# Kernel tuning notes

Hardware: AMD Instinct MI355X
Metric: run time of the kernel (lower is better)

## Reference

```python
import jax, jax.numpy as jnp
import numpy as np

B = 1024      # batch
E = 1024      # encoding_dim
OUT = 34      # 17 joints x 2 coords


def setup_inputs() -> dict:
    key = jax.random.key(0)
    ks = jax.random.split(key, 8)
    s = 0.02  # weight init scale
    return {
        "h": jax.random.normal(ks[0], (B, E), dtype=jnp.float32),
        "c": jax.random.normal(ks[1], (B, E), dtype=jnp.float32),
        "W_ih": jax.random.normal(ks[2], (4 * E, E), dtype=jnp.float32) * s,
        "W_hh": jax.random.normal(ks[3], (4 * E, E), dtype=jnp.float32) * s,
        "b_ih": jax.random.normal(ks[4], (4 * E,), dtype=jnp.float32) * s,
        "b_hh": jax.random.normal(ks[5], (4 * E,), dtype=jnp.float32) * s,
        "W_out": jax.random.normal(ks[6], (OUT, E), dtype=jnp.float32) * s,
        "b_out": jax.random.normal(ks[7], (OUT,), dtype=jnp.float32) * s,
        "future_preds": 10,
    }


def reference(h, c, W_ih, W_hh, b_ih, b_hh, W_out, b_out, future_preds):
    E_ = h.shape[1]
    start = jnp.zeros_like(h)  # zeros=True start token

    def step(carry, _):
        h_t, c_t, x = carry
        # LSTMCell: gates in PyTorch order i, f, g, o
        gates = x @ W_ih.T + b_ih + h_t @ W_hh.T + b_hh  # [B, 4E]
        i = jax.nn.sigmoid(gates[:, 0 * E_:1 * E_])
        f = jax.nn.sigmoid(gates[:, 1 * E_:2 * E_])
        g = jnp.tanh(gates[:, 2 * E_:3 * E_])
        o = jax.nn.sigmoid(gates[:, 3 * E_:4 * E_])
        c_new = f * c_t + i * g
        h_new = o * jnp.tanh(c_new)
        return (h_new, c_new, h_new), h_new

    _, hs = jax.lax.scan(step, (h, c, start), None, length=future_preds)
    # hs: [T, B, E] -> [B, T, E]
    preds = jnp.transpose(hs, (1, 0, 2))
    return preds @ W_out.T + b_out  # [B, T, 34]
```

## Files before the change

kernel.cpp:

```cpp
#include <hip/hip_runtime.h>
#include <cstdint>
#include <cstddef>

#define E_DIM   1024
#define B_DIM   1024
#define T_STEPS 10
#define OUT_DIM 34
#define OUT_PAD 48
#define HSTR    24
#define EK      128
#define WE_ELEMS (64 * EK)
#define DYN_LDS (2 * WE_ELEMS * 2 + 128 * HSTR * 2)
#define LDP     40

typedef __attribute__((ext_vector_type(4))) float  f32x4;
typedef __attribute__((ext_vector_type(8))) __bf16 bf16x8;

__device__ __forceinline__ unsigned short f2bf(float f) {
    unsigned int u = __float_as_uint(f);
    u = (u + 0x7FFFu + ((u >> 16) & 1u)) >> 16;
    return (unsigned short)u;
}
__device__ __forceinline__ float sigmoid_(float x) { return 1.0f / (1.0f + __expf(-x)); }
__device__ __forceinline__ float tanh_(float x)    { return 2.0f / (1.0f + __expf(-2.0f * x)) - 1.0f; }

__global__ void prep_weights_frag(const float* __restrict__ W_ih, const float* __restrict__ W_hh,
                                  unsigned short* __restrict__ WsumF, unsigned short* __restrict__ WhhF) {
    const int bn = blockIdx.x >> 3, E = blockIdx.x & 7;
    const int nt = threadIdx.x >> 6, lane = threadIdx.x & 63;
    const int j = lane & 15, q = lane >> 4;
    const int srow = nt * E_DIM + bn * 16 + j;
    const float* wi = W_ih + (size_t)srow * E_DIM;
    const float* wh = W_hh + (size_t)srow * E_DIM;
    const size_t dstb = (size_t)bn * 65536 + (size_t)E * 8192 + nt * 512 + lane * 8;
#pragma unroll
    for (int ks8 = 0; ks8 < 4; ++ks8) {
        const int k = E * 128 + ks8 * 32 + q * 8;
        float4 i0 = *(const float4*)(wi + k);
        float4 i1 = *(const float4*)(wi + k + 4);
        float4 h0 = *(const float4*)(wh + k);
        float4 h1 = *(const float4*)(wh + k + 4);
        unsigned short s[8], hh[8];
        s[0] = f2bf(i0.x + h0.x); s[1] = f2bf(i0.y + h0.y);
        s[2] = f2bf(i0.z + h0.z); s[3] = f2bf(i0.w + h0.w);
        s[4] = f2bf(i1.x + h1.x); s[5] = f2bf(i1.y + h1.y);
        s[6] = f2bf(i1.z + h1.z); s[7] = f2bf(i1.w + h1.w);
        hh[0] = f2bf(h0.x); hh[1] = f2bf(h0.y); hh[2] = f2bf(h0.z); hh[3] = f2bf(h0.w);
        hh[4] = f2bf(h1.x); hh[5] = f2bf(h1.y); hh[6] = f2bf(h1.z); hh[7] = f2bf(h1.w);
        *(uint4*)(WsumF + dstb + ks8 * 2048) = *(const uint4*)s;
        *(uint4*)(WhhF  + dstb + ks8 * 2048) = *(const uint4*)hh;
    }
}

__global__ void prep_state(const float* __restrict__ h0, const float* __restrict__ W_out,
                           const float* __restrict__ b_ih, const float* __restrict__ b_hh,
                           unsigned short* __restrict__ hbuf, unsigned short* __restrict__ Woutp,
                           float* __restrict__ bperm) {
    const int b = blockIdx.x;
    const int t = threadIdx.x;
    if (b < 1024) {
        const size_t i = ((size_t)b * 256 + t) * 4;
        float4 hv = *(const float4*)(h0 + i);
        hbuf[i + 0] = f2bf(hv.x);
        hbuf[i + 1] = f2bf(hv.y);
        hbuf[i + 2] = f2bf(hv.z);
        hbuf[i + 3] = f2bf(hv.w);
    } else if (b < 1072) {
        const int o = b - 1024;
        const int k = t * 4;
        float4 w = make_float4(0.f, 0.f, 0.f, 0.f);
        if (o < OUT_DIM) w = *(const float4*)(W_out + (size_t)o * E_DIM + k);
        const size_t dst = (size_t)o * E_DIM + k;
        Woutp[dst + 0] = f2bf(w.x);
        Woutp[dst + 1] = f2bf(w.y);
        Woutp[dst + 2] = f2bf(w.z);
        Woutp[dst + 3] = f2bf(w.w);
    } else {
        const int n = (b - 1072) * 256 + t;
        const int g = (n >> 4) & 3;
        const int e = ((n >> 6) << 4) | (n & 15);
        const int srow = g * E_DIM + e;
        bperm[n] = b_ih[srow] + b_hh[srow];
    }
}

__global__ void prep_c(const float* __restrict__ c0, float* __restrict__ C) {
    const int m = blockIdx.x;
    const int e0 = threadIdx.x * 4;
    float4 v = *(const float4*)(c0 + (size_t)m * E_DIM + e0);
    const int bm = m >> 7, wave = (m >> 5) & 3, mt = (m >> 4) & 1, q = (m >> 2) & 3, r = m & 3;
    const float vv[4] = {v.x, v.y, v.z, v.w};
#pragma unroll
    for (int ii = 0; ii < 4; ++ii) {
        const int e = e0 + ii;
        const int bn = e >> 4, j = e & 15;
        const int lane = q * 16 + j;
        C[(((size_t)(bn * 8 + bm) * 4 + wave) * 64 + lane) * 8 + mt * 4 + r] = vv[ii];
    }
}

__global__ __launch_bounds__(256, 2) void lstm_step(
    const unsigned short* __restrict__ WF,
    const float* __restrict__ bp,
    const unsigned short* __restrict__ Hin,
    float* __restrict__ C,
    unsigned short* __restrict__ Hout)
{
    extern __shared__ __align__(16) unsigned short smem[];
    unsigned short* Wb[2] = { smem, smem + WE_ELEMS };
    unsigned short* Ht    = smem + 2 * WE_ELEMS;

    const int tid  = threadIdx.x;
    const int wave = tid >> 6;
    const int lane = tid & 63;
    const int bn = blockIdx.x;
    const int bm = blockIdx.y;
    const int j  = lane & 15;
    const int q  = lane >> 4;

    f32x4 acc[2][4];
#pragma unroll
    for (int a = 0; a < 2; ++a)
#pragma unroll
        for (int b = 0; b < 4; ++b) acc[a][b] = (f32x4){0.f, 0.f, 0.f, 0.f};

    const int nb = bn * 64 + j;
    const float bi = bp[nb +  0];
    const float bf = bp[nb + 16];
    const float bg = bp[nb + 32];
    const float bo = bp[nb + 48];
    const size_t cbase = (((size_t)(bn * 8 + bm) * 4 + wave) * 64 + lane) * 8;
    float4 cold0 = *(const float4*)(C + cbase);
    float4 cold1 = *(const float4*)(C + cbase + 4);

    const unsigned short* arow0 = Hin + (size_t)(bm * 128 + wave * 32 + j) * E_DIM + q * 8;
    const unsigned short* arow1 = arow0 + (size_t)16 * E_DIM;
    const unsigned short* wsrc  = WF + (size_t)bn * 65536;

    uint4 ra[2][4][2];
    uint4 wreg[4];

#pragma unroll
    for (int s = 0; s < 4; ++s) {
        ra[0][s][0] = *(const uint4*)(arow0 + s * 32);
        ra[0][s][1] = *(const uint4*)(arow1 + s * 32);
    }
#pragma unroll
    for (int i = 0; i < 4; ++i)
        wreg[i] = *(const uint4*)(wsrc + (i * 256 + tid) * 8);
#pragma unroll
    for (int i = 0; i < 4; ++i)
        *(uint4*)(Wb[0] + (i * 256 + tid) * 8) = wreg[i];
    __syncthreads();

#pragma unroll
    for (int E = 0; E < 8; ++E) {
        const int cur = E & 1;
        if (E < 7) {
#pragma unroll
            for (int s = 0; s < 4; ++s) {
                ra[1 - cur][s][0] = *(const uint4*)(arow0 + (E + 1) * EK + s * 32);
                ra[1 - cur][s][1] = *(const uint4*)(arow1 + (E + 1) * EK + s * 32);
            }
#pragma unroll
            for (int i = 0; i < 4; ++i)
                wreg[i] = *(const uint4*)(wsrc + (size_t)(E + 1) * WE_ELEMS + (i * 256 + tid) * 8);
        }
        const unsigned short* wb = Wb[cur] + lane * 8;
#pragma unroll
        for (int ks8 = 0; ks8 < 4; ++ks8) {
            bf16x8 av0 = __builtin_bit_cast(bf16x8, ra[cur][ks8][0]);
            bf16x8 av1 = __builtin_bit_cast(bf16x8, ra[cur][ks8][1]);
            bf16x8 bv[4];
#pragma unroll
            for (int nt = 0; nt < 4; ++nt)
                bv[nt] = *(const bf16x8*)(wb + (ks8 * 4 + nt) * 512);
#pragma unroll
            for (int nt = 0; nt < 4; ++nt) {
                acc[0][nt] = __builtin_amdgcn_mfma_f32_16x16x32_bf16(av0, bv[nt], acc[0][nt], 0, 0, 0);
                acc[1][nt] = __builtin_amdgcn_mfma_f32_16x16x32_bf16(av1, bv[nt], acc[1][nt], 0, 0, 0);
            }
        }
        if (E < 7) {
            unsigned short* wn_ = Wb[1 - cur];
#pragma unroll
            for (int i = 0; i < 4; ++i)
                *(uint4*)(wn_ + (i * 256 + tid) * 8) = wreg[i];
            __syncthreads();
        }
    }

    float4 cnew[2];
    const float coldv[2][4] = {{cold0.x, cold0.y, cold0.z, cold0.w},
                               {cold1.x, cold1.y, cold1.z, cold1.w}};
#pragma unroll
    for (int mt = 0; mt < 2; ++mt) {
#pragma unroll
        for (int r = 0; r < 4; ++r) {
            const float iv = sigmoid_(acc[mt][0][r] + bi);
            const float fv = sigmoid_(acc[mt][1][r] + bf);
            const float gv = tanh_(acc[mt][2][r] + bg);
            const float ov = sigmoid_(acc[mt][3][r] + bo);
            const float cn = fv * coldv[mt][r] + iv * gv;
            cnew[mt][r] = cn;
            const int rowl = wave * 32 + mt * 16 + q * 4 + r;
            Ht[rowl * HSTR + j] = f2bf(ov * tanh_(cn));
        }
    }
    *(float4*)(C + cbase)     = cnew[0];
    *(float4*)(C + cbase + 4) = cnew[1];
    __syncthreads();

    {
        const int row = tid >> 1, part = tid & 1;
        uint4 v = *(const uint4*)(Ht + row * HSTR + part * 8);
        *(uint4*)(Hout + (size_t)(bm * 128 + row) * E_DIM + bn * 16 + part * 8) = v;
    }
}

__global__ __launch_bounds__(256) void proj_kernel(
    const unsigned short* __restrict__ Hs,
    const unsigned short* __restrict__ Wo,
    const float* __restrict__ b_out,
    float* __restrict__ Out)
{
    __shared__ float red[4][32][OUT_PAD];

    const int tid = threadIdx.x, wave = tid >> 6, lane = tid & 63;
    const int j = lane & 15, q = lane >> 4;
    const int t  = blockIdx.y;
    const int bb = blockIdx.x;
    const unsigned short* Hbase = Hs + ((size_t)t * B_DIM + (size_t)bb * 32) * E_DIM;
    const int k0 = wave * 256;

    f32x4 acc[2][3];
#pragma unroll
    for (int a = 0; a < 2; ++a)
#pragma unroll
        for (int b = 0; b < 3; ++b) acc[a][b] = (f32x4){0.f, 0.f, 0.f, 0.f};

#pragma unroll
    for (int kk = 0; kk < 256; kk += 32) {
        const int kc = k0 + kk + q * 8;
        bf16x8 av[2], bv[3];
#pragma unroll
        for (int mt = 0; mt < 2; ++mt)
            av[mt] = *(const bf16x8*)(Hbase + (size_t)(mt * 16 + j) * E_DIM + kc);
#pragma unroll
        for (int nt = 0; nt < 3; ++nt)
            bv[nt] = *(const bf16x8*)(Wo + (size_t)(nt * 16 + j) * E_DIM + kc);
#pragma unroll
        for (int mt = 0; mt < 2; ++mt)
#pragma unroll
            for (int nt = 0; nt < 3; ++nt)
                acc[mt][nt] = __builtin_amdgcn_mfma_f32_16x16x32_bf16(av[mt], bv[nt], acc[mt][nt], 0, 0, 0);
    }

#pragma unroll
    for (int mt = 0; mt < 2; ++mt)
#pragma unroll
        for (int nt = 0; nt < 3; ++nt)
#pragma unroll
            for (int r = 0; r < 4; ++r)
                red[wave][mt * 16 + q * 4 + r][nt * 16 + j] = acc[mt][nt][r];
    __syncthreads();

#pragma unroll
    for (int ii = 0; ii < 6; ++ii) {
        const int idx = tid * 6 + ii;
        const int row = idx / OUT_PAD, o = idx % OUT_PAD;
        if (o < OUT_DIM) {
            const float s = red[0][row][o] + red[1][row][o] + red[2][row][o] + red[3][row][o];
            Out[((size_t)(bb * 32 + row) * T_STEPS + t) * OUT_DIM + o] = s + b_out[o];
        }
    }
}

extern "C" void kernel_launch(void* const* d_in, const int* in_sizes, int n_in,
                              void* d_out, int out_size, void* d_ws, size_t ws_size,
                              hipStream_t stream) {
    (void)in_sizes; (void)n_in; (void)out_size; (void)ws_size;
    const float* h     = (const float*)d_in[0];
    const float* c     = (const float*)d_in[1];
    const float* W_ih  = (const float*)d_in[2];
    const float* W_hh  = (const float*)d_in[3];
    const float* b_ih  = (const float*)d_in[4];
    const float* b_hh  = (const float*)d_in[5];
    const float* W_out = (const float*)d_in[6];
    const float* b_out = (const float*)d_in[7];
    float* out = (float*)d_out;

    char* ws = (char*)d_ws;
    unsigned short* WsumF = (unsigned short*)(ws + 0);
    unsigned short* WhhF  = (unsigned short*)(ws + 8388608);
    float*          bperm = (float*)(ws + 16777216);
    unsigned short* Woutp = (unsigned short*)(ws + 16842752);
    float*          cbuf  = (float*)(ws + 16941056);
    unsigned short* hs    = (unsigned short*)(ws + 21135360);

    prep_weights_frag<<<512, 256, 0, stream>>>(W_ih, W_hh, WsumF, WhhF);
    prep_state<<<1088, 256, 0, stream>>>(h, W_out, b_ih, b_hh, hs, Woutp, bperm);
    prep_c<<<1024, 256, 0, stream>>>(c, cbuf);

    lstm_step<<<dim3(64, 8), 256, DYN_LDS, stream>>>(WhhF, bperm, hs, cbuf,
                                                     hs + (size_t)B_DIM * E_DIM);
    for (int t = 1; t < T_STEPS; ++t)
        lstm_step<<<dim3(64, 8), 256, DYN_LDS, stream>>>(WsumF, bperm,
                                                         hs + (size_t)t * B_DIM * E_DIM,
                                                         cbuf,
                                                         hs + (size_t)(t + 1) * B_DIM * E_DIM);

    proj_kernel<<<dim3(32, T_STEPS), 256, 0, stream>>>(hs + (size_t)B_DIM * E_DIM,
                                                       Woutp, b_out, out);
}
```

Baseline: 330.8 us.

## Retile LSTM step to 64x128 blocks with 8 waves and LDS gate exchange

Changes the LSTM step kernel from 128-row by 64-column tiles with 4 waves to 64-row by 128-column tiles (32 hidden units across all four gates) with 8 waves arranged 2x4. Gate accumulators are exchanged through LDS so the elementwise cell update reads C and writes H in natural row-major layout. This replaces the custom C permutation kernel with a plain device copy and the permuted bias with a summed bias. The weight prep kernel is rewritten to stage through LDS for the new fragment layout. Weight reuse per block and the grid shape change, and the bigger LDS footprint and extra barrier may limit occupancy.

```diff
diff --git a/kernel.cpp b/kernel.cpp
--- a/kernel.cpp
+++ b/kernel.cpp
@@ -7,11 +7,9 @@
 #define T_STEPS 10
 #define OUT_DIM 34
 #define OUT_PAD 48
-#define HSTR    24
 #define EK      128
-#define WE_ELEMS (64 * EK)
-#define DYN_LDS (2 * WE_ELEMS * 2 + 128 * HSTR * 2)
-#define LDP     40
+#define WSL_ELEMS (128 * EK)
+#define DYN_LDS (2 * WSL_ELEMS * 2)
 
 typedef __attribute__((ext_vector_type(4))) float  f32x4;
 typedef __attribute__((ext_vector_type(8))) __bf16 bf16x8;
@@ -24,38 +22,66 @@
 __device__ __forceinline__ float sigmoid_(float x) { return 1.0f / (1.0f + __expf(-x)); }
 __device__ __forceinline__ float tanh_(float x)    { return 2.0f / (1.0f + __expf(-2.0f * x)) - 1.0f; }
 
-__global__ void prep_weights_frag(const float* __restrict__ W_ih, const float* __restrict__ W_hh,
-                                  unsigned short* __restrict__ WsumF, unsigned short* __restrict__ WhhF) {
-    const int bn = blockIdx.x >> 3, E = blockIdx.x & 7;
-    const int nt = threadIdx.x >> 6, lane = threadIdx.x & 63;
-    const int j = lane & 15, q = lane >> 4;
-    const int srow = nt * E_DIM + bn * 16 + j;
-    const float* wi = W_ih + (size_t)srow * E_DIM;
-    const float* wh = W_hh + (size_t)srow * E_DIM;
-    const size_t dstb = (size_t)bn * 65536 + (size_t)E * 8192 + nt * 512 + lane * 8;
-#pragma unroll
-    for (int ks8 = 0; ks8 < 4; ++ks8) {
-        const int k = E * 128 + ks8 * 32 + q * 8;
-        float4 i0 = *(const float4*)(wi + k);
-        float4 i1 = *(const float4*)(wi + k + 4);
-        float4 h0 = *(const float4*)(wh + k);
-        float4 h1 = *(const float4*)(wh + k + 4);
-        unsigned short s[8], hh[8];
-        s[0] = f2bf(i0.x + h0.x); s[1] = f2bf(i0.y + h0.y);
-        s[2] = f2bf(i0.z + h0.z); s[3] = f2bf(i0.w + h0.w);
-        s[4] = f2bf(i1.x + h1.x); s[5] = f2bf(i1.y + h1.y);
-        s[6] = f2bf(i1.z + h1.z); s[7] = f2bf(i1.w + h1.w);
-        hh[0] = f2bf(h0.x); hh[1] = f2bf(h0.y); hh[2] = f2bf(h0.z); hh[3] = f2bf(h0.w);
-        hh[4] = f2bf(h1.x); hh[5] = f2bf(h1.y); hh[6] = f2bf(h1.z); hh[7] = f2bf(h1.w);
-        *(uint4*)(WsumF + dstb + ks8 * 2048) = *(const uint4*)s;
-        *(uint4*)(WhhF  + dstb + ks8 * 2048) = *(const uint4*)hh;
+__global__ __launch_bounds__(512) void prep_weights_frag(
+    const float* __restrict__ W_ih, const float* __restrict__ W_hh,
+    unsigned short* __restrict__ WsumF, unsigned short* __restrict__ WhhF) {
+    __shared__ unsigned short Ls[128 * 136];
+
+    const int bn2 = blockIdx.x >> 3, E8 = blockIdx.x & 7;
+    const int tid = threadIdx.x;
+
+    const int rl = tid >> 2, s = tid & 3;
+    const int sub_r = rl >> 4, jr = rl & 15;
+    const int g_r  = 2 * ((sub_r >> 1) & 1) + (sub_r & 1);
+    const int eb_r = 2 * bn2 + (sub_r >> 2);
+    const size_t grow = ((size_t)g_r * E_DIM + eb_r * 16 + jr) * E_DIM + E8 * 128;
+    unsigned short hhreg[32];
+#pragma unroll
+    for (int u = 0; u < 8; ++u) {
+        const int kl = u * 16 + s * 4;
+        float4 wi = *(const float4*)(W_ih + grow + kl);
+        float4 wh = *(const float4*)(W_hh + grow + kl);
+        Ls[rl * 136 + kl + 0] = f2bf(wi.x + wh.x);
+        Ls[rl * 136 + kl + 1] = f2bf(wi.y + wh.y);
+        Ls[rl * 136 + kl + 2] = f2bf(wi.z + wh.z);
+        Ls[rl * 136 + kl + 3] = f2bf(wi.w + wh.w);
+        hhreg[u * 4 + 0] = f2bf(wh.x);
+        hhreg[u * 4 + 1] = f2bf(wh.y);
+        hhreg[u * 4 + 2] = f2bf(wh.z);
+        hhreg[u * 4 + 3] = f2bf(wh.w);
+    }
+    __syncthreads();
+    const size_t dstb = (size_t)bn2 * 131072 + (size_t)E8 * 16384;
+#pragma unroll
+    for (int i = 0; i < 4; ++i) {
+        const int u4 = i * 512 + tid;
+        const int ks8 = u4 >> 9, sb = (u4 >> 6) & 7, ln = u4 & 63;
+        const int row = sb * 16 + (ln & 15), kl = ks8 * 32 + (ln >> 4) * 8;
+        *(uint4*)(WsumF + dstb + (size_t)u4 * 8) = *(const uint4*)(Ls + row * 136 + kl);
+    }
+    __syncthreads();
+#pragma unroll
+    for (int u = 0; u < 8; ++u) {
+        const int kl = u * 16 + s * 4;
+        Ls[rl * 136 + kl + 0] = hhreg[u * 4 + 0];
+        Ls[rl * 136 + kl + 1] = hhreg[u * 4 + 1];
+        Ls[rl * 136 + kl + 2] = hhreg[u * 4 + 2];
+        Ls[rl * 136 + kl + 3] = hhreg[u * 4 + 3];
+    }
+    __syncthreads();
+#pragma unroll
+    for (int i = 0; i < 4; ++i) {
+        const int u4 = i * 512 + tid;
+        const int ks8 = u4 >> 9, sb = (u4 >> 6) & 7, ln = u4 & 63;
+        const int row = sb * 16 + (ln & 15), kl = ks8 * 32 + (ln >> 4) * 8;
+        *(uint4*)(WhhF + dstb + (size_t)u4 * 8) = *(const uint4*)(Ls + row * 136 + kl);
     }
 }
 
 __global__ void prep_state(const float* __restrict__ h0, const float* __restrict__ W_out,
                            const float* __restrict__ b_ih, const float* __restrict__ b_hh,
                            unsigned short* __restrict__ hbuf, unsigned short* __restrict__ Woutp,
-                           float* __restrict__ bperm) {
+                           float* __restrict__ bsum) {
     const int b = blockIdx.x;
     const int t = threadIdx.x;
     if (b < 1024) {
@@ -77,144 +103,150 @@
         Woutp[dst + 3] = f2bf(w.w);
     } else {
         const int n = (b - 1072) * 256 + t;
-        const int g = (n >> 4) & 3;
-        const int e = ((n >> 6) << 4) | (n & 15);
-        const int srow = g * E_DIM + e;
-        bperm[n] = b_ih[srow] + b_hh[srow];
-    }
-}
-
-__global__ void prep_c(const float* __restrict__ c0, float* __restrict__ C) {
-    const int m = blockIdx.x;
-    const int e0 = threadIdx.x * 4;
-    float4 v = *(const float4*)(c0 + (size_t)m * E_DIM + e0);
-    const int bm = m >> 7, wave = (m >> 5) & 3, mt = (m >> 4) & 1, q = (m >> 2) & 3, r = m & 3;
-    const float vv[4] = {v.x, v.y, v.z, v.w};
-#pragma unroll
-    for (int ii = 0; ii < 4; ++ii) {
-        const int e = e0 + ii;
-        const int bn = e >> 4, j = e & 15;
-        const int lane = q * 16 + j;
-        C[(((size_t)(bn * 8 + bm) * 4 + wave) * 64 + lane) * 8 + mt * 4 + r] = vv[ii];
-    }
-}
-
-__global__ __launch_bounds__(256, 2) void lstm_step(
+        bsum[n] = b_ih[n] + b_hh[n];
+    }
+}
+
+__global__ __launch_bounds__(512, 4) void lstm_step(
     const unsigned short* __restrict__ WF,
-    const float* __restrict__ bp,
+    const float* __restrict__ bsum,
     const unsigned short* __restrict__ Hin,
     float* __restrict__ C,
     unsigned short* __restrict__ Hout)
 {
     extern __shared__ __align__(16) unsigned short smem[];
-    unsigned short* Wb[2] = { smem, smem + WE_ELEMS };
-    unsigned short* Ht    = smem + 2 * WE_ELEMS;
+    unsigned short* Wb[2] = { smem, smem + WSL_ELEMS };
 
     const int tid  = threadIdx.x;
     const int wave = tid >> 6;
     const int lane = tid & 63;
-    const int bn = blockIdx.x;
-    const int bm = blockIdx.y;
+    const int bn2 = blockIdx.x;
+    const int bm  = blockIdx.y;
+    const int wm = wave >> 2;
+    const int wn = wave & 3;
     const int j  = lane & 15;
     const int q  = lane >> 4;
 
-    f32x4 acc[2][4];
+    f32x4 acc[2][2];
 #pragma unroll
     for (int a = 0; a < 2; ++a)
 #pragma unroll
-        for (int b = 0; b < 4; ++b) acc[a][b] = (f32x4){0.f, 0.f, 0.f, 0.f};
-
-    const int nb = bn * 64 + j;
-    const float bi = bp[nb +  0];
-    const float bf = bp[nb + 16];
-    const float bg = bp[nb + 32];
-    const float bo = bp[nb + 48];
-    const size_t cbase = (((size_t)(bn * 8 + bm) * 4 + wave) * 64 + lane) * 8;
-    float4 cold0 = *(const float4*)(C + cbase);
-    float4 cold1 = *(const float4*)(C + cbase + 4);
-
-    const unsigned short* arow0 = Hin + (size_t)(bm * 128 + wave * 32 + j) * E_DIM + q * 8;
+        for (int b = 0; b < 2; ++b) acc[a][b] = (f32x4){0.f, 0.f, 0.f, 0.f};
+
+    const unsigned short* arow0 = Hin + (size_t)(bm * 64 + wm * 32 + j) * E_DIM + q * 8;
     const unsigned short* arow1 = arow0 + (size_t)16 * E_DIM;
-    const unsigned short* wsrc  = WF + (size_t)bn * 65536;
-
-    uint4 ra[2][4][2];
-    uint4 wreg[4];
-
-#pragma unroll
-    for (int s = 0; s < 4; ++s) {
+    const unsigned short* wsrc  = WF + (size_t)bn2 * 131072;
+
+    uint4 ra[2][2][2];
+#pragma unroll
+    for (int s = 0; s < 2; ++s) {
         ra[0][s][0] = *(const uint4*)(arow0 + s * 32);
         ra[0][s][1] = *(const uint4*)(arow1 + s * 32);
     }
+    uint4 wreg[4];
 #pragma unroll
     for (int i = 0; i < 4; ++i)
-        wreg[i] = *(const uint4*)(wsrc + (i * 256 + tid) * 8);
+        wreg[i] = *(const uint4*)(wsrc + (i * 512 + tid) * 8);
 #pragma unroll
     for (int i = 0; i < 4; ++i)
-        *(uint4*)(Wb[0] + (i * 256 + tid) * 8) = wreg[i];
-    __syncthreads();
-
-#pragma unroll
-    for (int E = 0; E < 8; ++E) {
-        const int cur = E & 1;
-        if (E < 7) {
-#pragma unroll
-            for (int s = 0; s < 4; ++s) {
-                ra[1 - cur][s][0] = *(const uint4*)(arow0 + (E + 1) * EK + s * 32);
-                ra[1 - cur][s][1] = *(const uint4*)(arow1 + (E + 1) * EK + s * 32);
+        *(uint4*)(Wb[0] + (i * 512 + tid) * 8) = wreg[i];
+    __syncthreads();
+
+    const int wboff = wn * 1024 + lane * 8;
+
+#pragma unroll
+    for (int E8 = 0; E8 < 8; ++E8) {
+        const unsigned short* wb = Wb[E8 & 1] + wboff;
+        if (E8 < 7) {
+#pragma unroll
+            for (int i = 0; i < 4; ++i)
+                wreg[i] = *(const uint4*)(wsrc + (size_t)(E8 + 1) * WSL_ELEMS + (i * 512 + tid) * 8);
+        }
+#pragma unroll
+        for (int ch = 0; ch < 2; ++ch) {
+            const int ci  = E8 * 2 + ch;
+            const int cur = ci & 1;
+            const int gi0 = ci * 2;
+            if (gi0 + 2 < 32) {
+#pragma unroll
+                for (int s = 0; s < 2; ++s) {
+                    ra[1 - cur][s][0] = *(const uint4*)(arow0 + (gi0 + 2 + s) * 32);
+                    ra[1 - cur][s][1] = *(const uint4*)(arow1 + (gi0 + 2 + s) * 32);
+                }
             }
 #pragma unroll
+            for (int s = 0; s < 2; ++s) {
+                const int ks8 = ch * 2 + s;
+                bf16x8 av0 = __builtin_bit_cast(bf16x8, ra[cur][s][0]);
+                bf16x8 av1 = __builtin_bit_cast(bf16x8, ra[cur][s][1]);
+                bf16x8 bv0 = *(const bf16x8*)(wb + ks8 * 4096);
+                bf16x8 bv1 = *(const bf16x8*)(wb + ks8 * 4096 + 512);
+                acc[0][0] = __builtin_amdgcn_mfma_f32_16x16x32_bf16(av0, bv0, acc[0][0], 0, 0, 0);
+                acc[0][1] = __builtin_amdgcn_mfma_f32_16x16x32_bf16(av0, bv1, acc[0][1], 0, 0, 0);
+                acc[1][0] = __builtin_amdgcn_mfma_f32_16x16x32_bf16(av1, bv0, acc[1][0], 0, 0, 0);
+                acc[1][1] = __builtin_amdgcn_mfma_f32_16x16x32_bf16(av1, bv1, acc[1][1], 0, 0, 0);
+            }
+        }
+        if (E8 < 7) {
+            unsigned short* wn_ = Wb[(E8 + 1) & 1];
+#pragma unroll
             for (int i = 0; i < 4; ++i)
-                wreg[i] = *(const uint4*)(wsrc + (size_t)(E + 1) * WE_ELEMS + (i * 256 + tid) * 8);
-        }
-        const unsigned short* wb = Wb[cur] + lane * 8;
-#pragma unroll
-        for (int ks8 = 0; ks8 < 4; ++ks8) {
-            bf16x8 av0 = __builtin_bit_cast(bf16x8, ra[cur][ks8][0]);
-            bf16x8 av1 = __builtin_bit_cast(bf16x8, ra[cur][ks8][1]);
-            bf16x8 bv[4];
-#pragma unroll
-            for (int nt = 0; nt < 4; ++nt)
-                bv[nt] = *(const bf16x8*)(wb + (ks8 * 4 + nt) * 512);
-#pragma unroll
-            for (int nt = 0; nt < 4; ++nt) {
-                acc[0][nt] = __builtin_amdgcn_mfma_f32_16x16x32_bf16(av0, bv[nt], acc[0][nt], 0, 0, 0);
-                acc[1][nt] = __builtin_amdgcn_mfma_f32_16x16x32_bf16(av1, bv[nt], acc[1][nt], 0, 0, 0);
+                *(uint4*)(wn_ + (i * 512 + tid) * 8) = wreg[i];
+            __syncthreads();
+        }
+    }
+
+    __syncthreads();
+    float* Gb = (float*)smem;
+    {
+        const int gp = wn & 1, ebl = wn >> 1;
+#pragma unroll
+        for (int mt = 0; mt < 2; ++mt)
+#pragma unroll
+            for (int nt = 0; nt < 2; ++nt) {
+                const int gate = 2 * gp + nt;
+                const int el = ebl * 16 + j;
+#pragma unroll
+                for (int r = 0; r < 4; ++r) {
+                    const int ml = wm * 32 + mt * 16 + q * 4 + r;
+                    Gb[(gate * 64 + ml) * 32 + el] = acc[mt][nt][r];
+                }
             }
-        }
-        if (E < 7) {
-            unsigned short* wn_ = Wb[1 - cur];
-#pragma unroll
-            for (int i = 0; i < 4; ++i)
-                *(uint4*)(wn_ + (i * 256 + tid) * 8) = wreg[i];
-            __syncthreads();
-        }
-    }
-
-    float4 cnew[2];
-    const float coldv[2][4] = {{cold0.x, cold0.y, cold0.z, cold0.w},
-                               {cold1.x, cold1.y, cold1.z, cold1.w}};
-#pragma unroll
-    for (int mt = 0; mt < 2; ++mt) {
-#pragma unroll
-        for (int r = 0; r < 4; ++r) {
-            const float iv = sigmoid_(acc[mt][0][r] + bi);
-            const float fv = sigmoid_(acc[mt][1][r] + bf);
-            const float gv = tanh_(acc[mt][2][r] + bg);
-            const float ov = sigmoid_(acc[mt][3][r] + bo);
-            const float cn = fv * coldv[mt][r] + iv * gv;
-            cnew[mt][r] = cn;
-            const int rowl = wave * 32 + mt * 16 + q * 4 + r;
-            Ht[rowl * HSTR + j] = f2bf(ov * tanh_(cn));
-        }
-    }
-    *(float4*)(C + cbase)     = cnew[0];
-    *(float4*)(C + cbase + 4) = cnew[1];
-    __syncthreads();
-
+    }
+    __syncthreads();
     {
-        const int row = tid >> 1, part = tid & 1;
-        uint4 v = *(const uint4*)(Ht + row * HSTR + part * 8);
-        *(uint4*)(Hout + (size_t)(bm * 128 + row) * E_DIM + bn * 16 + part * 8) = v;
+        const int ml = tid >> 3;
+        const int e4 = (tid & 7) * 4;
+        const int mg = bm * 64 + ml;
+        const int eg = bn2 * 32 + e4;
+        float4 vi = *(const float4*)(Gb + (0 * 64 + ml) * 32 + e4);
+        float4 vf = *(const float4*)(Gb + (1 * 64 + ml) * 32 + e4);
+        float4 vg = *(const float4*)(Gb + (2 * 64 + ml) * 32 + e4);
+        float4 vo = *(const float4*)(Gb + (3 * 64 + ml) * 32 + e4);
+        float4 bi = *(const float4*)(bsum + 0 * E_DIM + eg);
+        float4 bf = *(const float4*)(bsum + 1 * E_DIM + eg);
+        float4 bg = *(const float4*)(bsum + 2 * E_DIM + eg);
+        float4 bo = *(const float4*)(bsum + 3 * E_DIM + eg);
+        const size_t cidx = (size_t)mg * E_DIM + eg;
+        float4 cold = *(const float4*)(C + cidx);
+        float cn[4]; unsigned short hb[4];
+        const float iv_[4] = {vi.x + bi.x, vi.y + bi.y, vi.z + bi.z, vi.w + bi.w};
+        const float fv_[4] = {vf.x + bf.x, vf.y + bf.y, vf.z + bf.z, vf.w + bf.w};
+        const float gv_[4] = {vg.x + bg.x, vg.y + bg.y, vg.z + bg.z, vg.w + bg.w};
+        const float ov_[4] = {vo.x + bo.x, vo.y + bo.y, vo.z + bo.z, vo.w + bo.w};
+        const float co_[4] = {cold.x, cold.y, cold.z, cold.w};
+#pragma unroll
+        for (int i = 0; i < 4; ++i) {
+            const float iv = sigmoid_(iv_[i]);
+            const float fv = sigmoid_(fv_[i]);
+            const float gv = tanh_(gv_[i]);
+            const float ov = sigmoid_(ov_[i]);
+            const float c2 = fv * co_[i] + iv * gv;
+            cn[i] = c2;
+            hb[i] = f2bf(ov * tanh_(c2));
+        }
+        *(float4*)(C + cidx) = make_float4(cn[0], cn[1], cn[2], cn[3]);
+        *(uint2*)(Hout + cidx) = *(const uint2*)hb;
     }
 }
 
@@ -293,22 +325,26 @@
     char* ws = (char*)d_ws;
     unsigned short* WsumF = (unsigned short*)(ws + 0);
     unsigned short* WhhF  = (unsigned short*)(ws + 8388608);
-    float*          bperm = (float*)(ws + 16777216);
+    float*          bsum  = (float*)(ws + 16777216);
     unsigned short* Woutp = (unsigned short*)(ws + 16842752);
     float*          cbuf  = (float*)(ws + 16941056);
     unsigned short* hs    = (unsigned short*)(ws + 21135360);
 
-    prep_weights_frag<<<512, 256, 0, stream>>>(W_ih, W_hh, WsumF, WhhF);
-    prep_state<<<1088, 256, 0, stream>>>(h, W_out, b_ih, b_hh, hs, Woutp, bperm);
-    prep_c<<<1024, 256, 0, stream>>>(c, cbuf);
-
-    lstm_step<<<dim3(64, 8), 256, DYN_LDS, stream>>>(WhhF, bperm, hs, cbuf,
-                                                     hs + (size_t)B_DIM * E_DIM);
+    hipFuncSetAttribute((const void*)lstm_step,
+                        hipFuncAttributeMaxDynamicSharedMemorySize, DYN_LDS);
+
+    prep_weights_frag<<<256, 512, 0, stream>>>(W_ih, W_hh, WsumF, WhhF);
+    prep_state<<<1088, 256, 0, stream>>>(h, W_out, b_ih, b_hh, hs, Woutp, bsum);
+    hipMemcpyAsync(cbuf, c, (size_t)B_DIM * E_DIM * sizeof(float),
+                   hipMemcpyDeviceToDevice, stream);
+
+    lstm_step<<<dim3(32, 16), 512, DYN_LDS, stream>>>(WhhF, bsum, hs, cbuf,
+                                                      hs + (size_t)B_DIM * E_DIM);
     for (int t = 1; t < T_STEPS; ++t)
-        lstm_step<<<dim3(64, 8), 256, DYN_LDS, stream>>>(WsumF, bperm,
-                                                         hs + (size_t)t * B_DIM * E_DIM,
-                                                         cbuf,
-                                                         hs + (size_t)(t + 1) * B_DIM * E_DIM);
+        lstm_step<<<dim3(32, 16), 512, DYN_LDS, stream>>>(WsumF, bsum,
+                                                          hs + (size_t)t * B_DIM * E_DIM,
+                                                          cbuf,
+                                                          hs + (size_t)(t + 1) * B_DIM * E_DIM);
 
     proj_kernel<<<dim3(32, T_STEPS), 256, 0, stream>>>(hs + (size_t)B_DIM * E_DIM,
                                                        Woutp, b_out, out);
```

New measurement: 469.9 us. 1.42x slower.

## Halve LSTM step M-tile, split waves over gates, and stage gates through LDS

Applied to the files above, without the earlier changes.

Each lstm_step block now covers 64 batch rows instead of 128, giving a 64x16 grid, with the four waves arranged 2x2 over rows and gate pairs. Gate pre-activations are staged through LDS so the pointwise LSTM update runs with coalesced row-major cell-state and h accesses. This removes the custom cell-state layout and its prep kernel, which is replaced by a plain device-to-device copy. The change aims for more blocks and higher occupancy (launch bounds raised to 4 blocks per SM) on a latency-bound recurrence, at the cost of reading each weight tile twice as often and adding an extra LDS round trip and barrier.

```diff
diff --git a/kernel.cpp b/kernel.cpp
--- a/kernel.cpp
+++ b/kernel.cpp
@@ -7,11 +7,10 @@
 #define T_STEPS 10
 #define OUT_DIM 34
 #define OUT_PAD 48
-#define HSTR    24
 #define EK      128
 #define WE_ELEMS (64 * EK)
-#define DYN_LDS (2 * WE_ELEMS * 2 + 128 * HSTR * 2)
-#define LDP     40
+#define GSTR    20
+#define DYN_LDS (2 * WE_ELEMS * 2)
 
 typedef __attribute__((ext_vector_type(4))) float  f32x4;
 typedef __attribute__((ext_vector_type(8))) __bf16 bf16x8;
@@ -84,22 +83,7 @@
     }
 }
 
-__global__ void prep_c(const float* __restrict__ c0, float* __restrict__ C) {
-    const int m = blockIdx.x;
-    const int e0 = threadIdx.x * 4;
-    float4 v = *(const float4*)(c0 + (size_t)m * E_DIM + e0);
-    const int bm = m >> 7, wave = (m >> 5) & 3, mt = (m >> 4) & 1, q = (m >> 2) & 3, r = m & 3;
-    const float vv[4] = {v.x, v.y, v.z, v.w};
-#pragma unroll
-    for (int ii = 0; ii < 4; ++ii) {
-        const int e = e0 + ii;
-        const int bn = e >> 4, j = e & 15;
-        const int lane = q * 16 + j;
-        C[(((size_t)(bn * 8 + bm) * 4 + wave) * 64 + lane) * 8 + mt * 4 + r] = vv[ii];
-    }
-}
-
-__global__ __launch_bounds__(256, 2) void lstm_step(
+__global__ __launch_bounds__(256, 4) void lstm_step(
     const unsigned short* __restrict__ WF,
     const float* __restrict__ bp,
     const unsigned short* __restrict__ Hin,
@@ -108,43 +92,34 @@
 {
     extern __shared__ __align__(16) unsigned short smem[];
     unsigned short* Wb[2] = { smem, smem + WE_ELEMS };
-    unsigned short* Ht    = smem + 2 * WE_ELEMS;
 
     const int tid  = threadIdx.x;
     const int wave = tid >> 6;
     const int lane = tid & 63;
     const int bn = blockIdx.x;
     const int bm = blockIdx.y;
+    const int wm  = wave >> 1;
+    const int wn2 = wave & 1;
     const int j  = lane & 15;
     const int q  = lane >> 4;
 
-    f32x4 acc[2][4];
+    f32x4 acc[2][2];
 #pragma unroll
     for (int a = 0; a < 2; ++a)
 #pragma unroll
-        for (int b = 0; b < 4; ++b) acc[a][b] = (f32x4){0.f, 0.f, 0.f, 0.f};
-
-    const int nb = bn * 64 + j;
-    const float bi = bp[nb +  0];
-    const float bf = bp[nb + 16];
-    const float bg = bp[nb + 32];
-    const float bo = bp[nb + 48];
-    const size_t cbase = (((size_t)(bn * 8 + bm) * 4 + wave) * 64 + lane) * 8;
-    float4 cold0 = *(const float4*)(C + cbase);
-    float4 cold1 = *(const float4*)(C + cbase + 4);
-
-    const unsigned short* arow0 = Hin + (size_t)(bm * 128 + wave * 32 + j) * E_DIM + q * 8;
+        for (int b = 0; b < 2; ++b) acc[a][b] = (f32x4){0.f, 0.f, 0.f, 0.f};
+
+    const unsigned short* arow0 = Hin + (size_t)(bm * 64 + wm * 32 + j) * E_DIM + q * 8;
     const unsigned short* arow1 = arow0 + (size_t)16 * E_DIM;
     const unsigned short* wsrc  = WF + (size_t)bn * 65536;
 
     uint4 ra[2][4][2];
-    uint4 wreg[4];
-
 #pragma unroll
     for (int s = 0; s < 4; ++s) {
         ra[0][s][0] = *(const uint4*)(arow0 + s * 32);
         ra[0][s][1] = *(const uint4*)(arow1 + s * 32);
     }
+    uint4 wreg[4];
 #pragma unroll
     for (int i = 0; i < 4; ++i)
         wreg[i] = *(const uint4*)(wsrc + (i * 256 + tid) * 8);
@@ -153,35 +128,34 @@
         *(uint4*)(Wb[0] + (i * 256 + tid) * 8) = wreg[i];
     __syncthreads();
 
-#pragma unroll
-    for (int E = 0; E < 8; ++E) {
-        const int cur = E & 1;
-        if (E < 7) {
+    const int wboff = wn2 * 1024 + lane * 8;
+
+#pragma unroll
+    for (int E8 = 0; E8 < 8; ++E8) {
+        const int cur = E8 & 1;
+        const unsigned short* wb = Wb[cur] + wboff;
+        if (E8 < 7) {
 #pragma unroll
             for (int s = 0; s < 4; ++s) {
-                ra[1 - cur][s][0] = *(const uint4*)(arow0 + (E + 1) * EK + s * 32);
-                ra[1 - cur][s][1] = *(const uint4*)(arow1 + (E + 1) * EK + s * 32);
+                ra[1 - cur][s][0] = *(const uint4*)(arow0 + (E8 + 1) * EK + s * 32);
+                ra[1 - cur][s][1] = *(const uint4*)(arow1 + (E8 + 1) * EK + s * 32);
             }
 #pragma unroll
             for (int i = 0; i < 4; ++i)
-                wreg[i] = *(const uint4*)(wsrc + (size_t)(E + 1) * WE_ELEMS + (i * 256 + tid) * 8);
-        }
-        const unsigned short* wb = Wb[cur] + lane * 8;
+                wreg[i] = *(const uint4*)(wsrc + (size_t)(E8 + 1) * WE_ELEMS + (i * 256 + tid) * 8);
+        }
 #pragma unroll
         for (int ks8 = 0; ks8 < 4; ++ks8) {
             bf16x8 av0 = __builtin_bit_cast(bf16x8, ra[cur][ks8][0]);
             bf16x8 av1 = __builtin_bit_cast(bf16x8, ra[cur][ks8][1]);
-            bf16x8 bv[4];
-#pragma unroll
-            for (int nt = 0; nt < 4; ++nt)
-                bv[nt] = *(const bf16x8*)(wb + (ks8 * 4 + nt) * 512);
-#pragma unroll
-            for (int nt = 0; nt < 4; ++nt) {
-                acc[0][nt] = __builtin_amdgcn_mfma_f32_16x16x32_bf16(av0, bv[nt], acc[0][nt], 0, 0, 0);
-                acc[1][nt] = __builtin_amdgcn_mfma_f32_16x16x32_bf16(av1, bv[nt], acc[1][nt], 0, 0, 0);
-            }
-        }
-        if (E < 7) {
+            bf16x8 bv0 = *(const bf16x8*)(wb + ks8 * 2048);
+            bf16x8 bv1 = *(const bf16x8*)(wb + ks8 * 2048 + 512);
+            acc[0][0] = __builtin_amdgcn_mfma_f32_16x16x32_bf16(av0, bv0, acc[0][0], 0, 0, 0);
+            acc[0][1] = __builtin_amdgcn_mfma_f32_16x16x32_bf16(av0, bv1, acc[0][1], 0, 0, 0);
+            acc[1][0] = __builtin_amdgcn_mfma_f32_16x16x32_bf16(av1, bv0, acc[1][0], 0, 0, 0);
+            acc[1][1] = __builtin_amdgcn_mfma_f32_16x16x32_bf16(av1, bv1, acc[1][1], 0, 0, 0);
+        }
+        if (E8 < 7) {
             unsigned short* wn_ = Wb[1 - cur];
 #pragma unroll
             for (int i = 0; i < 4; ++i)
@@ -190,31 +164,53 @@
         }
     }
 
-    float4 cnew[2];
-    const float coldv[2][4] = {{cold0.x, cold0.y, cold0.z, cold0.w},
-                               {cold1.x, cold1.y, cold1.z, cold1.w}};
-#pragma unroll
-    for (int mt = 0; mt < 2; ++mt) {
-#pragma unroll
-        for (int r = 0; r < 4; ++r) {
-            const float iv = sigmoid_(acc[mt][0][r] + bi);
-            const float fv = sigmoid_(acc[mt][1][r] + bf);
-            const float gv = tanh_(acc[mt][2][r] + bg);
-            const float ov = sigmoid_(acc[mt][3][r] + bo);
-            const float cn = fv * coldv[mt][r] + iv * gv;
-            cnew[mt][r] = cn;
-            const int rowl = wave * 32 + mt * 16 + q * 4 + r;
-            Ht[rowl * HSTR + j] = f2bf(ov * tanh_(cn));
-        }
-    }
-    *(float4*)(C + cbase)     = cnew[0];
-    *(float4*)(C + cbase + 4) = cnew[1];
     __syncthreads();
-
+    float* Gb = (float*)smem;
     {
-        const int row = tid >> 1, part = tid & 1;
-        uint4 v = *(const uint4*)(Ht + row * HSTR + part * 8);
-        *(uint4*)(Hout + (size_t)(bm * 128 + row) * E_DIM + bn * 16 + part * 8) = v;
+#pragma unroll
+        for (int mt = 0; mt < 2; ++mt)
+#pragma unroll
+            for (int nt = 0; nt < 2; ++nt) {
+                const int gate = wn2 * 2 + nt;
+#pragma unroll
+                for (int r = 0; r < 4; ++r) {
+                    const int ml = wm * 32 + mt * 16 + q * 4 + r;
+                    Gb[(gate * 64 + ml) * GSTR + j] = acc[mt][nt][r];
+                }
+            }
+    }
+    __syncthreads();
+    {
+        const int ml = tid >> 2;
+        const int e4 = (tid & 3) * 4;
+        float4 vi = *(const float4*)(Gb + (0 * 64 + ml) * GSTR + e4);
+        float4 vf = *(const float4*)(Gb + (1 * 64 + ml) * GSTR + e4);
+        float4 vg = *(const float4*)(Gb + (2 * 64 + ml) * GSTR + e4);
+        float4 vo = *(const float4*)(Gb + (3 * 64 + ml) * GSTR + e4);
+        float4 bi = *(const float4*)(bp + bn * 64 +  0 + e4);
+        float4 bf = *(const float4*)(bp + bn * 64 + 16 + e4);
+        float4 bg = *(const float4*)(bp + bn * 64 + 32 + e4);
+        float4 bo = *(const float4*)(bp + bn * 64 + 48 + e4);
+        const size_t cidx = (size_t)(bm * 64 + ml) * E_DIM + bn * 16 + e4;
+        float4 cold = *(const float4*)(C + cidx);
+        float cn[4]; unsigned short hb[4];
+        const float iv_[4] = {vi.x + bi.x, vi.y + bi.y, vi.z + bi.z, vi.w + bi.w};
+        const float fv_[4] = {vf.x + bf.x, vf.y + bf.y, vf.z + bf.z, vf.w + bf.w};
+        const float gv_[4] = {vg.x + bg.x, vg.y + bg.y, vg.z + bg.z, vg.w + bg.w};
+        const float ov_[4] = {vo.x + bo.x, vo.y + bo.y, vo.z + bo.z, vo.w + bo.w};
+        const float co_[4] = {cold.x, cold.y, cold.z, cold.w};
+#pragma unroll
+        for (int i = 0; i < 4; ++i) {
+            const float iv = sigmoid_(iv_[i]);
+            const float fv = sigmoid_(fv_[i]);
+            const float gv = tanh_(gv_[i]);
+            const float ov = sigmoid_(ov_[i]);
+            const float c2 = fv * co_[i] + iv * gv;
+            cn[i] = c2;
+            hb[i] = f2bf(ov * tanh_(c2));
+        }
+        *(float4*)(C + cidx) = make_float4(cn[0], cn[1], cn[2], cn[3]);
+        *(uint2*)(Hout + cidx) = *(const uint2*)hb;
     }
 }
 
@@ -298,17 +294,21 @@
     float*          cbuf  = (float*)(ws + 16941056);
     unsigned short* hs    = (unsigned short*)(ws + 21135360);
 
+    hipFuncSetAttribute((const void*)lstm_step,
+                        hipFuncAttributeMaxDynamicSharedMemorySize, DYN_LDS);
+
     prep_weights_frag<<<512, 256, 0, stream>>>(W_ih, W_hh, WsumF, WhhF);
     prep_state<<<1088, 256, 0, stream>>>(h, W_out, b_ih, b_hh, hs, Woutp, bperm);
-    prep_c<<<1024, 256, 0, stream>>>(c, cbuf);
-
-    lstm_step<<<dim3(64, 8), 256, DYN_LDS, stream>>>(WhhF, bperm, hs, cbuf,
-                                                     hs + (size_t)B_DIM * E_DIM);
+    hipMemcpyAsync(cbuf, c, (size_t)B_DIM * E_DIM * sizeof(float),
+                   hipMemcpyDeviceToDevice, stream);
+
+    lstm_step<<<dim3(64, 16), 256, DYN_LDS, stream>>>(WhhF, bperm, hs, cbuf,
+                                                      hs + (size_t)B_DIM * E_DIM);
     for (int t = 1; t < T_STEPS; ++t)
-        lstm_step<<<dim3(64, 8), 256, DYN_LDS, stream>>>(WsumF, bperm,
-                                                         hs + (size_t)t * B_DIM * E_DIM,
-                                                         cbuf,
-                                                         hs + (size_t)(t + 1) * B_DIM * E_DIM);
+        lstm_step<<<dim3(64, 16), 256, DYN_LDS, stream>>>(WsumF, bperm,
+                                                          hs + (size_t)t * B_DIM * E_DIM,
+                                                          cbuf,
+                                                          hs + (size_t)(t + 1) * B_DIM * E_DIM);
 
     proj_kernel<<<dim3(32, T_STEPS), 256, 0, stream>>>(hs + (size_t)B_DIM * E_DIM,
                                                        Woutp, b_out, out);
```

After: 469.5 us. 1.42x slower.

## Widen LSTM step tile to 128x128 with 8 waves in a 4x2 grid

Applied to the files above, without the earlier changes.

Each lstm_step block now covers 32 hidden units (128 gate columns) with 512 threads arranged as 4 M-waves by 2 N-waves, instead of 16 units with 256 threads. The weight fragment layout, bias permutation and cell-state layout are re-indexed to match, and the grid halves to 32x8 blocks. The aim is to halve how often each A (h) tile is re-read from global memory across blocks, and to reuse the weight LDS buffer for the output staging. The cost is a larger LDS footprint (64KB), which needs the max dynamic shared memory attribute, fewer blocks to fill the CUs, and higher register pressure under launch bounds of 512 threads with 2 blocks.

```diff
diff --git a/kernel.cpp b/kernel.cpp
--- a/kernel.cpp
+++ b/kernel.cpp
@@ -7,11 +7,11 @@
 #define T_STEPS 10
 #define OUT_DIM 34
 #define OUT_PAD 48
-#define HSTR    24
 #define EK      128
-#define WE_ELEMS (64 * EK)
-#define DYN_LDS (2 * WE_ELEMS * 2 + 128 * HSTR * 2)
-#define LDP     40
+#define WE_ELEMS (128 * EK)
+#define SLICE_ELEMS (8 * WE_ELEMS)
+#define HSTR    48
+#define DYN_LDS (2 * WE_ELEMS * 2)
 
 typedef __attribute__((ext_vector_type(4))) float  f32x4;
 typedef __attribute__((ext_vector_type(8))) __bf16 bf16x8;
@@ -24,18 +24,20 @@
 __device__ __forceinline__ float sigmoid_(float x) { return 1.0f / (1.0f + __expf(-x)); }
 __device__ __forceinline__ float tanh_(float x)    { return 2.0f / (1.0f + __expf(-2.0f * x)) - 1.0f; }
 
-__global__ void prep_weights_frag(const float* __restrict__ W_ih, const float* __restrict__ W_hh,
-                                  unsigned short* __restrict__ WsumF, unsigned short* __restrict__ WhhF) {
-    const int bn = blockIdx.x >> 3, E = blockIdx.x & 7;
-    const int nt = threadIdx.x >> 6, lane = threadIdx.x & 63;
+__global__ __launch_bounds__(512) void prep_weights_frag(
+    const float* __restrict__ W_ih, const float* __restrict__ W_hh,
+    unsigned short* __restrict__ WsumF, unsigned short* __restrict__ WhhF) {
+    const int bn = blockIdx.x >> 3, E8 = blockIdx.x & 7;
+    const int sub = threadIdx.x >> 6, lane = threadIdx.x & 63;
     const int j = lane & 15, q = lane >> 4;
-    const int srow = nt * E_DIM + bn * 16 + j;
-    const float* wi = W_ih + (size_t)srow * E_DIM;
-    const float* wh = W_hh + (size_t)srow * E_DIM;
-    const size_t dstb = (size_t)bn * 65536 + (size_t)E * 8192 + nt * 512 + lane * 8;
+    const int g = sub & 3;
+    const int e = bn * 32 + ((sub >> 2) << 4) + j;
+    const float* wi = W_ih + ((size_t)g * E_DIM + e) * E_DIM;
+    const float* wh = W_hh + ((size_t)g * E_DIM + e) * E_DIM;
+    const size_t dstb = (size_t)bn * SLICE_ELEMS + (size_t)E8 * WE_ELEMS + sub * 512 + lane * 8;
 #pragma unroll
     for (int ks8 = 0; ks8 < 4; ++ks8) {
-        const int k = E * 128 + ks8 * 32 + q * 8;
+        const int k = E8 * 128 + ks8 * 32 + q * 8;
         float4 i0 = *(const float4*)(wi + k);
         float4 i1 = *(const float4*)(wi + k + 4);
         float4 h0 = *(const float4*)(wh + k);
@@ -47,8 +49,8 @@
         s[6] = f2bf(i1.z + h1.z); s[7] = f2bf(i1.w + h1.w);
         hh[0] = f2bf(h0.x); hh[1] = f2bf(h0.y); hh[2] = f2bf(h0.z); hh[3] = f2bf(h0.w);
         hh[4] = f2bf(h1.x); hh[5] = f2bf(h1.y); hh[6] = f2bf(h1.z); hh[7] = f2bf(h1.w);
-        *(uint4*)(WsumF + dstb + ks8 * 2048) = *(const uint4*)s;
-        *(uint4*)(WhhF  + dstb + ks8 * 2048) = *(const uint4*)hh;
+        *(uint4*)(WsumF + dstb + ks8 * 4096) = *(const uint4*)s;
+        *(uint4*)(WhhF  + dstb + ks8 * 4096) = *(const uint4*)hh;
     }
 }
 
@@ -77,10 +79,10 @@
         Woutp[dst + 3] = f2bf(w.w);
     } else {
         const int n = (b - 1072) * 256 + t;
-        const int g = (n >> 4) & 3;
-        const int e = ((n >> 6) << 4) | (n & 15);
-        const int srow = g * E_DIM + e;
-        bperm[n] = b_ih[srow] + b_hh[srow];
+        const int bn = n >> 7, sub = (n >> 4) & 7, j = n & 15;
+        const int g = sub & 3;
+        const int e = bn * 32 + ((sub >> 2) << 4) + j;
+        bperm[n] = b_ih[g * E_DIM + e] + b_hh[g * E_DIM + e];
     }
 }
 
@@ -88,18 +90,19 @@
     const int m = blockIdx.x;
     const int e0 = threadIdx.x * 4;
     float4 v = *(const float4*)(c0 + (size_t)m * E_DIM + e0);
-    const int bm = m >> 7, wave = (m >> 5) & 3, mt = (m >> 4) & 1, q = (m >> 2) & 3, r = m & 3;
+    const int bm = m >> 7, wm = (m >> 5) & 3, mt = (m >> 4) & 1, q = (m >> 2) & 3, r = m & 3;
     const float vv[4] = {v.x, v.y, v.z, v.w};
 #pragma unroll
     for (int ii = 0; ii < 4; ++ii) {
         const int e = e0 + ii;
-        const int bn = e >> 4, j = e & 15;
+        const int bn = e >> 5, wn = (e >> 4) & 1, j = e & 15;
+        const int wave = wm * 2 + wn;
         const int lane = q * 16 + j;
-        C[(((size_t)(bn * 8 + bm) * 4 + wave) * 64 + lane) * 8 + mt * 4 + r] = vv[ii];
-    }
-}
-
-__global__ __launch_bounds__(256, 2) void lstm_step(
+        C[(((size_t)(bn * 8 + bm) * 8 + wave) * 64 + lane) * 8 + mt * 4 + r] = vv[ii];
+    }
+}
+
+__global__ __launch_bounds__(512, 2) void lstm_step(
     const unsigned short* __restrict__ WF,
     const float* __restrict__ bp,
     const unsigned short* __restrict__ Hin,
@@ -108,13 +111,14 @@
 {
     extern __shared__ __align__(16) unsigned short smem[];
     unsigned short* Wb[2] = { smem, smem + WE_ELEMS };
-    unsigned short* Ht    = smem + 2 * WE_ELEMS;
 
     const int tid  = threadIdx.x;
     const int wave = tid >> 6;
     const int lane = tid & 63;
     const int bn = blockIdx.x;
     const int bm = blockIdx.y;
+    const int wm = wave >> 1;
+    const int wn = wave & 1;
     const int j  = lane & 15;
     const int q  = lane >> 4;
 
@@ -124,49 +128,50 @@
 #pragma unroll
         for (int b = 0; b < 4; ++b) acc[a][b] = (f32x4){0.f, 0.f, 0.f, 0.f};
 
-    const int nb = bn * 64 + j;
+    const int nb = bn * 128 + wn * 64 + j;
     const float bi = bp[nb +  0];
     const float bf = bp[nb + 16];
     const float bg = bp[nb + 32];
     const float bo = bp[nb + 48];
-    const size_t cbase = (((size_t)(bn * 8 + bm) * 4 + wave) * 64 + lane) * 8;
+    const size_t cbase = (((size_t)(bn * 8 + bm) * 8 + wave) * 64 + lane) * 8;
     float4 cold0 = *(const float4*)(C + cbase);
     float4 cold1 = *(const float4*)(C + cbase + 4);
 
-    const unsigned short* arow0 = Hin + (size_t)(bm * 128 + wave * 32 + j) * E_DIM + q * 8;
+    const unsigned short* arow0 = Hin + (size_t)(bm * 128 + wm * 32 + j) * E_DIM + q * 8;
     const unsigned short* arow1 = arow0 + (size_t)16 * E_DIM;
-    const unsigned short* wsrc  = WF + (size_t)bn * 65536;
+    const unsigned short* wsrc  = WF + (size_t)bn * SLICE_ELEMS;
 
     uint4 ra[2][4][2];
-    uint4 wreg[4];
-
 #pragma unroll
     for (int s = 0; s < 4; ++s) {
         ra[0][s][0] = *(const uint4*)(arow0 + s * 32);
         ra[0][s][1] = *(const uint4*)(arow1 + s * 32);
     }
+    uint4 wreg[4];
 #pragma unroll
     for (int i = 0; i < 4; ++i)
-        wreg[i] = *(const uint4*)(wsrc + (i * 256 + tid) * 8);
+        wreg[i] = *(const uint4*)(wsrc + (i * 512 + tid) * 8);
 #pragma unroll
     for (int i = 0; i < 4; ++i)
-        *(uint4*)(Wb[0] + (i * 256 + tid) * 8) = wreg[i];
+        *(uint4*)(Wb[0] + (i * 512 + tid) * 8) = wreg[i];
     __syncthreads();
 
-#pragma unroll
-    for (int E = 0; E < 8; ++E) {
-        const int cur = E & 1;
-        if (E < 7) {
+    const int wboff = wn * 2048 + lane * 8;
+
+#pragma unroll
+    for (int E8 = 0; E8 < 8; ++E8) {
+        const int cur = E8 & 1;
+        const unsigned short* wb = Wb[cur] + wboff;
+        if (E8 < 7) {
 #pragma unroll
             for (int s = 0; s < 4; ++s) {
-                ra[1 - cur][s][0] = *(const uint4*)(arow0 + (E + 1) * EK + s * 32);
-                ra[1 - cur][s][1] = *(const uint4*)(arow1 + (E + 1) * EK + s * 32);
+                ra[1 - cur][s][0] = *(const uint4*)(arow0 + (E8 + 1) * EK + s * 32);
+                ra[1 - cur][s][1] = *(const uint4*)(arow1 + (E8 + 1) * EK + s * 32);
             }
 #pragma unroll
             for (int i = 0; i < 4; ++i)
-                wreg[i] = *(const uint4*)(wsrc + (size_t)(E + 1) * WE_ELEMS + (i * 256 + tid) * 8);
-        }
-        const unsigned short* wb = Wb[cur] + lane * 8;
+                wreg[i] = *(const uint4*)(wsrc + (size_t)(E8 + 1) * WE_ELEMS + (i * 512 + tid) * 8);
+        }
 #pragma unroll
         for (int ks8 = 0; ks8 < 4; ++ks8) {
             bf16x8 av0 = __builtin_bit_cast(bf16x8, ra[cur][ks8][0]);
@@ -174,22 +179,24 @@
             bf16x8 bv[4];
 #pragma unroll
             for (int nt = 0; nt < 4; ++nt)
-                bv[nt] = *(const bf16x8*)(wb + (ks8 * 4 + nt) * 512);
+                bv[nt] = *(const bf16x8*)(wb + ks8 * 4096 + nt * 512);
 #pragma unroll
             for (int nt = 0; nt < 4; ++nt) {
                 acc[0][nt] = __builtin_amdgcn_mfma_f32_16x16x32_bf16(av0, bv[nt], acc[0][nt], 0, 0, 0);
                 acc[1][nt] = __builtin_amdgcn_mfma_f32_16x16x32_bf16(av1, bv[nt], acc[1][nt], 0, 0, 0);
             }
         }
-        if (E < 7) {
+        if (E8 < 7) {
             unsigned short* wn_ = Wb[1 - cur];
 #pragma unroll
             for (int i = 0; i < 4; ++i)
-                *(uint4*)(wn_ + (i * 256 + tid) * 8) = wreg[i];
+                *(uint4*)(wn_ + (i * 512 + tid) * 8) = wreg[i];
             __syncthreads();
         }
     }
 
+    __syncthreads();
+    unsigned short* Ht = smem;
     float4 cnew[2];
     const float coldv[2][4] = {{cold0.x, cold0.y, cold0.z, cold0.w},
                                {cold1.x, cold1.y, cold1.z, cold1.w}};
@@ -203,8 +210,8 @@
             const float ov = sigmoid_(acc[mt][3][r] + bo);
             const float cn = fv * coldv[mt][r] + iv * gv;
             cnew[mt][r] = cn;
-            const int rowl = wave * 32 + mt * 16 + q * 4 + r;
-            Ht[rowl * HSTR + j] = f2bf(ov * tanh_(cn));
+            const int rowl = wm * 32 + mt * 16 + q * 4 + r;
+            Ht[rowl * HSTR + wn * 16 + j] = f2bf(ov * tanh_(cn));
         }
     }
     *(float4*)(C + cbase)     = cnew[0];
@@ -212,9 +219,9 @@
     __syncthreads();
 
     {
-        const int row = tid >> 1, part = tid & 1;
-        uint4 v = *(const uint4*)(Ht + row * HSTR + part * 8);
-        *(uint4*)(Hout + (size_t)(bm * 128 + row) * E_DIM + bn * 16 + part * 8) = v;
+        const int row = tid >> 2, part = (tid & 3) * 8;
+        uint4 v = *(const uint4*)(Ht + row * HSTR + part);
+        *(uint4*)(Hout + (size_t)(bm * 128 + row) * E_DIM + bn * 32 + part) = v;
     }
 }
 
@@ -298,14 +305,17 @@
     float*          cbuf  = (float*)(ws + 16941056);
     unsigned short* hs    = (unsigned short*)(ws + 21135360);
 
-    prep_weights_frag<<<512, 256, 0, stream>>>(W_ih, W_hh, WsumF, WhhF);
+    hipFuncSetAttribute((const void*)lstm_step,
+                        hipFuncAttributeMaxDynamicSharedMemorySize, DYN_LDS);
+
+    prep_weights_frag<<<256, 512, 0, stream>>>(W_ih, W_hh, WsumF, WhhF);
     prep_state<<<1088, 256, 0, stream>>>(h, W_out, b_ih, b_hh, hs, Woutp, bperm);
     prep_c<<<1024, 256, 0, stream>>>(c, cbuf);
 
-    lstm_step<<<dim3(64, 8), 256, DYN_LDS, stream>>>(WhhF, bperm, hs, cbuf,
+    lstm_step<<<dim3(32, 8), 512, DYN_LDS, stream>>>(WhhF, bperm, hs, cbuf,
                                                      hs + (size_t)B_DIM * E_DIM);
     for (int t = 1; t < T_STEPS; ++t)
-        lstm_step<<<dim3(64, 8), 256, DYN_LDS, stream>>>(WsumF, bperm,
+        lstm_step<<<dim3(32, 8), 512, DYN_LDS, stream>>>(WsumF, bperm,
                                                          hs + (size_t)t * B_DIM * E_DIM,
                                                          cbuf,
                                                          hs + (size_t)(t + 1) * B_DIM * E_DIM);
```

Result: slower. 363.5 us (+9.9%).
